# Kernel optimization log

Hardware: AMD Instinct MI355X
Metric: run time of the kernel (lower is better)

## Reference

```python
import jax, jax.numpy as jnp
import numpy as np

NUM_CLASSES = 80
TOPK = 1000
CONF_THRESH = 0.001
NMS_THRESH = 0.5
CLASS_OFFSET = 4096.0  # > max image coordinate, separates classes for class-aware NMS
M = 300000


def setup_inputs() -> dict:
    key = jax.random.key(0)
    k1, k2, k3, k4 = jax.random.split(key, 4)
    obj_preds = jax.random.normal(k1, (1, M, 1), dtype=jnp.float32)
    cls_preds = jax.random.normal(k2, (1, M, NUM_CLASSES), dtype=jnp.float32)
    # random xyxy boxes inside a 640x640 image
    cxcy = jax.random.uniform(k3, (1, M, 2), dtype=jnp.float32) * 640.0
    wh = jax.random.uniform(k4, (1, M, 2), dtype=jnp.float32) * 128.0 + 1.0
    box_preds = jnp.concatenate([cxcy - wh * 0.5, cxcy + wh * 0.5], axis=-1)
    return {"obj_preds": obj_preds, "cls_preds": cls_preds, "box_preds": box_preds}


def _iou_matrix(boxes):
    # boxes: [K, 4] xyxy -> [K, K] pairwise IoU
    x1, y1, x2, y2 = boxes[:, 0], boxes[:, 1], boxes[:, 2], boxes[:, 3]
    area = jnp.clip(x2 - x1, 0.0) * jnp.clip(y2 - y1, 0.0)
    xx1 = jnp.maximum(x1[:, None], x1[None, :])
    yy1 = jnp.maximum(y1[:, None], y1[None, :])
    xx2 = jnp.minimum(x2[:, None], x2[None, :])
    yy2 = jnp.minimum(y2[:, None], y2[None, :])
    inter = jnp.clip(xx2 - xx1, 0.0) * jnp.clip(yy2 - yy1, 0.0)
    return inter / (area[:, None] + area[None, :] - inter + 1e-9)


def _postprocess(obj_preds, cls_preds, box_preds):
    obj = obj_preds[0]   # [M, 1]
    cls = cls_preds[0]   # [M, C]
    box = box_preds[0]   # [M, 4]

    # sigmoid * sigmoid sqrt-score fusion (no_multi_labels branch)
    fused = jnp.sqrt(jax.nn.sigmoid(obj) * jax.nn.sigmoid(cls))  # [M, C]
    scores = jnp.max(fused, axis=1)     # [M]
    labels = jnp.argmax(fused, axis=1)  # [M]

    # sort-descending + take top-k == lax.top_k
    topk_scores, topk_idxs = jax.lax.top_k(scores, TOPK)
    labels_k = labels[topk_idxs]        # [K]
    boxes_k = box[topk_idxs]            # [K, 4]
    conf_mask = topk_scores > CONF_THRESH

    # multiclass NMS via class-offset trick (boxes of different classes never overlap)
    off = labels_k.astype(boxes_k.dtype)[:, None] * CLASS_OFFSET
    iou = _iou_matrix(boxes_k + off)    # [K, K]

    idx = jnp.arange(TOPK)

    def body(i, keep):
        # suppressed if any earlier, still-kept box overlaps > nms_thresh
        sup = (iou[i] > NMS_THRESH) & keep & (idx < i)
        return keep.at[i].set(keep[i] & ~jnp.any(sup))

    keep = jax.lax.fori_loop(0, TOPK, body, conf_mask)  # [K] bool

    keepf = keep.astype(topk_scores.dtype)
    # fixed-shape output: masked [K, 5] = (score, x1, y1, x2, y2); dropped rows zeroed
    out5 = jnp.concatenate([(topk_scores * keepf)[:, None], boxes_k * keepf[:, None]], axis=1)
    return out5, labels_k, keep


def reference(obj_preds, cls_preds, box_preds):
    return _postprocess(obj_preds, cls_preds, box_preds)
```

## Files before the change

kernel.cpp:

```cpp
#include <hip/hip_runtime.h>
#include <hip/hip_bf16.h>
#include <math.h>

#define NCLS 80
#define TOPK_N 1000
#define CAND_CAP 12288
#define T0 0.91f
#define OBJ_T 1.55f
#define NB 8192
#define HREP 8
#define RBINS 3072
#define RBIN_LO 0x3F680000u
#define ANCH_INV 524287

#define WS_SCORES   0
#define WS_CAND     1200000
#define WS_TKSCORE  1298304
#define WS_TKANCH   1302304
#define WS_TKLABEL  1306304
#define WS_BOXES    1310304
#define WS_OBX      1326304
#define WS_AREAS    1342304
#define WS_MASK     1346304
#define WS_META     1474304
#define WS_HIST     1474368

typedef unsigned long long u64;

__device__ __forceinline__ float sigmoidf_(float x) {
    return 1.0f / (1.0f + expf(-x));
}

__device__ __forceinline__ u64 make_key2(unsigned s32, int anchor) {
    return ((u64)s32 << 19) | (unsigned)(ANCH_INV - anchor);
}

__device__ __forceinline__ int key_bin(u64 k) {
    unsigned s32 = (unsigned)(k >> 19);
    int d = (int)(s32 - RBIN_LO);
    if (d < 0) d = 0;
    int b = d >> 9;
    if (b > RBINS - 1) b = RBINS - 1;
    return (RBINS - 1) - b;
}

__device__ __forceinline__ void rowmax16(const float4* row, int l,
                                         float& bv, int& bc) {
    float4 v4 = row[l];
    bv = v4.x; bc = l * 4;
    if (v4.y > bv) { bv = v4.y; bc = l * 4 + 1; }
    if (v4.z > bv) { bv = v4.z; bc = l * 4 + 2; }
    if (v4.w > bv) { bv = v4.w; bc = l * 4 + 3; }
    if (l < 4) {
        float4 w4 = row[16 + l];
        int cb = 64 + l * 4;
        if (w4.x > bv) { bv = w4.x; bc = cb; }
        if (w4.y > bv) { bv = w4.y; bc = cb + 1; }
        if (w4.z > bv) { bv = w4.z; bc = cb + 2; }
        if (w4.w > bv) { bv = w4.w; bc = cb + 3; }
    }
    #pragma unroll
    for (int m = 8; m >= 1; m >>= 1) {
        float ov = __shfl_xor(bv, m);
        int oc = __shfl_xor(bc, m);
        if (ov > bv || (ov == bv && oc < bc)) { bv = ov; bc = oc; }
    }
}

__global__ void __launch_bounds__(256)
k1_scores(const float* __restrict__ obj,
          const float* __restrict__ cls,
          u64* __restrict__ cand,
          int* __restrict__ counter,
          unsigned* __restrict__ hist,
          int M) {
    __shared__ int lcount, lbase;
    __shared__ u64 lkeys[64];
    int t = threadIdx.x;
    if (t == 0) lcount = 0;
    if (blockIdx.x < 4096 && t < 4)
        ((uint4*)hist)[blockIdx.x * 4 + t] = make_uint4(0u, 0u, 0u, 0u);
    __syncthreads();
    int l = t & 15;
    int grp = t >> 4;
    int base = blockIdx.x * 64 + grp * 4;
    if (base < M) {
        float4 ov = *(const float4*)(obj + base);
        float o4[4] = {ov.x, ov.y, ov.z, ov.w};
        #pragma unroll
        for (int j = 0; j < 4; ++j) {
            float o = o4[j];
            if (o > OBJ_T) {
                int anchor = base + j;
                const float4* p = (const float4*)(cls + (size_t)anchor * NCLS);
                float4 v = p[l];
                float m = fmaxf(fmaxf(v.x, v.y), fmaxf(v.z, v.w));
                if (l < 4) {
                    float4 w4 = p[16 + l];
                    m = fmaxf(m, fmaxf(fmaxf(w4.x, w4.y), fmaxf(w4.z, w4.w)));
                }
                #pragma unroll
                for (int s = 8; s >= 1; s >>= 1)
                    m = fmaxf(m, __shfl_xor(m, s));
                if (l == 0) {
                    float score = sqrtf(sigmoidf_(o) * sigmoidf_(m));
                    if (score > T0) {
                        int pos = atomicAdd(&lcount, 1);
                        lkeys[pos] = make_key2(__float_as_uint(score), anchor);
                    }
                }
            }
        }
    }
    __syncthreads();
    if (t == 0 && lcount > 0) lbase = atomicAdd(counter, lcount);
    __syncthreads();
    int n = lcount;
    if (t < n) {
        int pos = lbase + t;
        if (pos < CAND_CAP) cand[pos] = lkeys[t];
    }
}

__global__ void kf_hist(const float* __restrict__ obj,
                        const float* __restrict__ cls,
                        float* __restrict__ scores,
                        unsigned* __restrict__ hist,
                        const int* __restrict__ meta, int M) {
    int C = meta[2];
    if (C >= TOPK_N && C <= CAND_CAP) return;
    int gw = (blockIdx.x * 256 + threadIdx.x) >> 6;
    int TW = gridDim.x * 4;
    int lane = threadIdx.x & 63;
    int g = lane >> 4, l = lane & 15;
    int rep = blockIdx.x & (HREP - 1);
    for (int a0 = gw * 4; a0 < M; a0 += TW * 4) {
        int anchor = a0 + g;
        if (anchor >= M) continue;
        const float4* row = (const float4*)(cls + (size_t)anchor * NCLS);
        float bv; int bc;
        rowmax16(row, l, bv, bc);
        if (l == 0) {
            float score = sqrtf(sigmoidf_(obj[anchor]) * sigmoidf_(bv));
            scores[anchor] = score;
            atomicAdd(&hist[(size_t)rep * NB + (__float_as_uint(score) >> 17)], 1u);
        }
    }
}

__global__ void k2_scan(const unsigned* __restrict__ hist, int* __restrict__ meta) {
    int C = meta[2];
    if (C >= TOPK_N && C <= CAND_CAP) return;
    int t = threadIdx.x;
    int lane = t & 63, w = t >> 6;
    int base = NB - 1 - t * 8;
    unsigned bins[8]; unsigned s = 0;
    #pragma unroll
    for (int k = 0; k < 8; ++k) {
        unsigned h = 0;
        for (int r = 0; r < HREP; ++r) h += hist[(size_t)r * NB + base - k];
        bins[k] = h; s += h;
    }
    unsigned inc = s;
    for (int d = 1; d < 64; d <<= 1) {
        unsigned pv = __shfl_up(inc, d);
        if (lane >= d) inc += pv;
    }
    __shared__ unsigned wsum[16], woff[16];
    if (lane == 63) wsum[w] = inc;
    __syncthreads();
    if (t == 0) {
        unsigned cum = 0;
        for (int i = 0; i < 16; ++i) { woff[i] = cum; cum += wsum[i]; }
    }
    __syncthreads();
    unsigned excl = woff[w] + inc - s;
    if (excl < TOPK_N && excl + s >= TOPK_N) {
        unsigned cum = excl; int b = base;
        #pragma unroll
        for (int k = 0; k < 8; ++k) {
            unsigned h = bins[k];
            if (cum + h >= TOPK_N) { meta[0] = b; break; }
            cum += h; --b;
        }
    }
}

__global__ void k3_compact(const float* __restrict__ scores,
                           int* __restrict__ meta,
                           u64* __restrict__ cand, int M) {
    int C = meta[2];
    if (C >= TOPK_N && C <= CAND_CAP) return;
    int B = meta[0];
    for (int i = blockIdx.x * 256 + threadIdx.x; i < M; i += gridDim.x * 256) {
        unsigned key = __float_as_uint(scores[i]);
        if ((int)(key >> 17) >= B) {
            int pos = atomicAdd(meta + 3, 1);
            if (pos < CAND_CAP)
                cand[pos] = make_key2(key, i);
        }
    }
}

__global__ void __launch_bounds__(1024)
k4_rank(const u64* __restrict__ cand,
        const int* __restrict__ meta,
        float* __restrict__ tkscore,
        int* __restrict__ tkanchor) {
    __shared__ u64 sorted[CAND_CAP];
    __shared__ unsigned hist[RBINS];
    __shared__ unsigned cnt[RBINS];
    __shared__ unsigned wsum[16], woff[16];
    int t = threadIdx.x;
    int lane = t & 63, w = t >> 6;
    int Cf = meta[2];
    bool fast = (Cf >= TOPK_N && Cf <= CAND_CAP);
    int C = fast ? Cf : meta[3];
    if (C > CAND_CAP) C = CAND_CAP;
    for (int b = t; b < RBINS; b += 1024) { hist[b] = 0; cnt[b] = 0; }
    __syncthreads();
    u64 keys[12]; int nk = 0;
    for (int i = t; i < C; i += 1024) {
        u64 k = cand[i];
        keys[nk++] = k;
        atomicAdd(&hist[key_bin(k)], 1u);
    }
    __syncthreads();
    unsigned h0 = hist[t * 3], h1 = hist[t * 3 + 1], h2 = hist[t * 3 + 2];
    unsigned s = h0 + h1 + h2;
    unsigned inc = s;
    for (int d = 1; d < 64; d <<= 1) {
        unsigned pv = __shfl_up(inc, d);
        if (lane >= d) inc += pv;
    }
    if (lane == 63) wsum[w] = inc;
    __syncthreads();
    if (t == 0) {
        unsigned cum = 0;
        for (int i = 0; i < 16; ++i) { woff[i] = cum; cum += wsum[i]; }
    }
    __syncthreads();
    unsigned base = woff[w] + inc - s;
    hist[t * 3] = base;
    hist[t * 3 + 1] = base + h0;
    hist[t * 3 + 2] = base + h0 + h1;
    __syncthreads();
    nk = 0;
    for (int i = t; i < C; i += 1024) {
        u64 k = keys[nk++];
        int b = key_bin(k);
        unsigned pos = hist[b] + atomicAdd(&cnt[b], 1u);
        sorted[pos] = k;
    }
    __syncthreads();
    for (int p = t; p < C; p += 1024) {
        u64 k = sorted[p];
        int b = key_bin(k);
        unsigned b0 = hist[b], b1 = b0 + cnt[b];
        int r = (int)b0;
        for (unsigned q = b0; q < b1; ++q) r += (sorted[q] > k);
        if (r < TOPK_N) {
            tkscore[r] = __uint_as_float((unsigned)(k >> 19));
            tkanchor[r] = ANCH_INV - (int)(k & 0x7FFFF);
        }
    }
}

__global__ void __launch_bounds__(256)
k4b_gather(const float* __restrict__ cls,
           const float4* __restrict__ box,
           const int* __restrict__ tkanchor,
           int* __restrict__ tklabel,
           float4* __restrict__ boxes_k,
           float4* __restrict__ obx,
           float* __restrict__ areas) {
    int grp = threadIdx.x >> 4, l = threadIdx.x & 15;
    int r = blockIdx.x * 16 + grp;
    if (r >= TOPK_N) return;
    int anchor = tkanchor[r];
    const float4* row = (const float4*)(cls + (size_t)anchor * NCLS);
    float bv; int bc;
    rowmax16(row, l, bv, bc);
    if (l == 0) {
        tklabel[r] = bc;
        float4 b = box[anchor];
        boxes_k[r] = b;
        float off = (float)bc * 4096.0f;
        float4 ob = make_float4(b.x + off, b.y + off, b.z + off, b.w + off);
        obx[r] = ob;
        areas[r] = fmaxf(ob.z - ob.x, 0.0f) * fmaxf(ob.w - ob.y, 0.0f);
    }
}

__global__ void k5_iou(const float4* __restrict__ obx,
                       const float* __restrict__ areas,
                       u64* __restrict__ mask) {
    int i = blockIdx.x * 4 + (threadIdx.x >> 6);
    int lane = threadIdx.x & 63;
    if (i >= TOPK_N) return;
    float4 bi = obx[i];
    float ai = areas[i];
    for (int w = 0; w < 16; ++w) {
        int c = w * 64 + lane;
        bool bit = false;
        if (c < i) {
            float4 bc = obx[c];
            float xx1 = fmaxf(bi.x, bc.x), yy1 = fmaxf(bi.y, bc.y);
            float xx2 = fminf(bi.z, bc.z), yy2 = fminf(bi.w, bc.w);
            float inter = fmaxf(xx2 - xx1, 0.0f) * fmaxf(yy2 - yy1, 0.0f);
            float iou = inter / (ai + areas[c] - inter + 1e-9f);
            bit = iou > 0.5f;
        }
        u64 bal = __ballot(bit);
        if (lane == 0) mask[(size_t)i * 16 + w] = bal;
    }
}

__global__ void __launch_bounds__(1024)
k6_nms(const float* __restrict__ tkscore,
       const u64* __restrict__ mask,
       const int* __restrict__ tklabel,
       const float4* __restrict__ boxes_k,
       float* __restrict__ out) {
    __shared__ u64 kept_s[16], dec_s[16];
    int t = threadIdx.x, w = t >> 6, lane = t & 63;
    bool active = t < TOPK_N;
    u64 sup[16];
    float sc = 0.0f;
    if (active) {
        #pragma unroll
        for (int q = 0; q < 16; ++q) sup[q] = mask[(size_t)t * 16 + q];
        sc = tkscore[t];
    } else {
        #pragma unroll
        for (int q = 0; q < 16; ++q) sup[q] = 0ULL;
    }
    bool conf = active && (sc > 0.001f);
    bool mydec = !conf;
    bool mykept = false;
    u64 db = __ballot(mydec), kb = __ballot(mykept);
    if (lane == 0) { dec_s[w] = db; kept_s[w] = kb; }
    __syncthreads();
    for (int round = 0; round < TOPK_N; ++round) {
        if (!mydec) {
            u64 pend = 0;
            #pragma unroll
            for (int q = 0; q < 16; ++q) pend |= sup[q] & ~dec_s[q];
            if (pend == 0ULL) {
                u64 kk = 0;
                #pragma unroll
                for (int q = 0; q < 16; ++q) kk |= sup[q] & kept_s[q];
                mydec = true; mykept = (kk == 0ULL);
            }
        }
        __syncthreads();
        db = __ballot(mydec); kb = __ballot(mykept);
        if (lane == 0) { dec_s[w] = db; kept_s[w] = kb; }
        __syncthreads();
        u64 a = ~0ULL;
        #pragma unroll
        for (int q = 0; q < 16; ++q) a &= dec_s[q];
        if (a == ~0ULL) break;
    }
    if (active) {
        float k = mykept ? 1.0f : 0.0f;
        float4 b = boxes_k[t];
        out[t * 5 + 0] = sc * k;
        out[t * 5 + 1] = b.x * k;
        out[t * 5 + 2] = b.y * k;
        out[t * 5 + 3] = b.z * k;
        out[t * 5 + 4] = b.w * k;
        out[5 * TOPK_N + t] = (float)tklabel[t];
        out[6 * TOPK_N + t] = k;
    }
}

extern "C" void kernel_launch(void* const* d_in, const int* in_sizes, int n_in,
                              void* d_out, int out_size, void* d_ws, size_t ws_size,
                              hipStream_t stream) {
    const float* obj = (const float*)d_in[0];
    const float* cls = (const float*)d_in[1];
    const float* box = (const float*)d_in[2];
    float* out = (float*)d_out;
    char* ws = (char*)d_ws;
    int M = in_sizes[0];

    float*    scores  = (float*)(ws + WS_SCORES);
    u64*      cand    = (u64*)(ws + WS_CAND);
    float*    tkscore = (float*)(ws + WS_TKSCORE);
    int*      tkanch  = (int*)(ws + WS_TKANCH);
    int*      tklabel = (int*)(ws + WS_TKLABEL);
    float4*   boxes_k = (float4*)(ws + WS_BOXES);
    float4*   obx     = (float4*)(ws + WS_OBX);
    float*    areas   = (float*)(ws + WS_AREAS);
    u64*      mask    = (u64*)(ws + WS_MASK);
    int*      meta    = (int*)(ws + WS_META);
    unsigned* hist    = (unsigned*)(ws + WS_HIST);

    hipMemsetAsync(ws + WS_META, 0, 64, stream);

    k1_scores<<<(M + 63) / 64, 256, 0, stream>>>(obj, cls, cand, meta + 2, hist, M);
    kf_hist<<<512, 256, 0, stream>>>(obj, cls, scores, hist, meta, M);
    k2_scan<<<1, 1024, 0, stream>>>(hist, meta);
    k3_compact<<<512, 256, 0, stream>>>(scores, meta, cand, M);
    k4_rank<<<1, 1024, 0, stream>>>(cand, meta, tkscore, tkanch);
    k4b_gather<<<(TOPK_N + 15) / 16, 256, 0, stream>>>(cls, (const float4*)box,
                                                       tkanch, tklabel, boxes_k, obx, areas);
    k5_iou<<<(TOPK_N + 3) / 4, 256, 0, stream>>>(obx, areas, mask);
    k6_nms<<<1, 1024, 0, stream>>>(tkscore, mask, tklabel, boxes_k, out);
}
```

Measured before the change: 191.4 us.

## Compact objectness survivors in k1 and fold histogram scan into kf_hist tail

k1_scores now runs one anchor per thread and gathers anchors whose objectness passes the threshold into shared memory. 16-lane groups then take only those survivors for the class-row max, and the grid shrinks to a quarter of the blocks. The separate k2_scan launch is removed: the last block of kf_hist, found with an atomic counter and threadfence, performs the histogram scan itself with 256 threads covering 32 bins each. This saves one kernel launch and raises lane utilization in the prefilter. The cost is a serial tail in the last block and atomic reads of the histogram.

```diff
diff --git a/kernel.cpp b/kernel.cpp
--- a/kernel.cpp
+++ b/kernel.cpp
@@ -74,41 +74,41 @@
           int* __restrict__ counter,
           unsigned* __restrict__ hist,
           int M) {
-    __shared__ int lcount, lbase;
-    __shared__ u64 lkeys[64];
+    __shared__ int lcount, lbase, nsurv;
+    __shared__ int sanch[256];
+    __shared__ float sobj[256];
+    __shared__ u64 lkeys[256];
     int t = threadIdx.x;
-    if (t == 0) lcount = 0;
-    if (blockIdx.x < 4096 && t < 4)
-        ((uint4*)hist)[blockIdx.x * 4 + t] = make_uint4(0u, 0u, 0u, 0u);
-    __syncthreads();
-    int l = t & 15;
-    int grp = t >> 4;
-    int base = blockIdx.x * 64 + grp * 4;
-    if (base < M) {
-        float4 ov = *(const float4*)(obj + base);
-        float o4[4] = {ov.x, ov.y, ov.z, ov.w};
+    if (t == 0) { lcount = 0; nsurv = 0; }
+    for (int i = blockIdx.x * 256 + t; i < (HREP * NB) / 4; i += gridDim.x * 256)
+        ((uint4*)hist)[i] = make_uint4(0u, 0u, 0u, 0u);
+    __syncthreads();
+    int a = blockIdx.x * 256 + t;
+    float o = (a < M) ? obj[a] : -1e30f;
+    if (o > OBJ_T) {
+        int p = atomicAdd(&nsurv, 1);
+        sanch[p] = a; sobj[p] = o;
+    }
+    __syncthreads();
+    int ns = nsurv;
+    int grp = t >> 4, l = t & 15;
+    for (int s = grp; s < ns; s += 16) {
+        int anchor = sanch[s];
+        const float4* p = (const float4*)(cls + (size_t)anchor * NCLS);
+        float4 v = p[l];
+        float m = fmaxf(fmaxf(v.x, v.y), fmaxf(v.z, v.w));
+        if (l < 4) {
+            float4 w4 = p[16 + l];
+            m = fmaxf(m, fmaxf(fmaxf(w4.x, w4.y), fmaxf(w4.z, w4.w)));
+        }
         #pragma unroll
-        for (int j = 0; j < 4; ++j) {
-            float o = o4[j];
-            if (o > OBJ_T) {
-                int anchor = base + j;
-                const float4* p = (const float4*)(cls + (size_t)anchor * NCLS);
-                float4 v = p[l];
-                float m = fmaxf(fmaxf(v.x, v.y), fmaxf(v.z, v.w));
-                if (l < 4) {
-                    float4 w4 = p[16 + l];
-                    m = fmaxf(m, fmaxf(fmaxf(w4.x, w4.y), fmaxf(w4.z, w4.w)));
-                }
-                #pragma unroll
-                for (int s = 8; s >= 1; s >>= 1)
-                    m = fmaxf(m, __shfl_xor(m, s));
-                if (l == 0) {
-                    float score = sqrtf(sigmoidf_(o) * sigmoidf_(m));
-                    if (score > T0) {
-                        int pos = atomicAdd(&lcount, 1);
-                        lkeys[pos] = make_key2(__float_as_uint(score), anchor);
-                    }
-                }
+        for (int sh = 8; sh >= 1; sh >>= 1)
+            m = fmaxf(m, __shfl_xor(m, sh));
+        if (l == 0) {
+            float score = sqrtf(sigmoidf_(sobj[s]) * sigmoidf_(m));
+            if (score > T0) {
+                int pos = atomicAdd(&lcount, 1);
+                lkeys[pos] = make_key2(__float_as_uint(score), anchor);
             }
         }
     }
@@ -126,13 +126,14 @@
                         const float* __restrict__ cls,
                         float* __restrict__ scores,
                         unsigned* __restrict__ hist,
-                        const int* __restrict__ meta, int M) {
+                        int* __restrict__ meta, int M) {
     int C = meta[2];
     if (C >= TOPK_N && C <= CAND_CAP) return;
-    int gw = (blockIdx.x * 256 + threadIdx.x) >> 6;
+    int t = threadIdx.x;
+    int gw = (blockIdx.x * 256 + t) >> 6;
     int TW = gridDim.x * 4;
-    int lane = threadIdx.x & 63;
-    int g = lane >> 4, l = lane & 15;
+    int lane64 = t & 63;
+    int g = lane64 >> 4, l = lane64 & 15;
     int rep = blockIdx.x & (HREP - 1);
     for (int a0 = gw * 4; a0 < M; a0 += TW * 4) {
         int anchor = a0 + g;
@@ -146,19 +147,20 @@
             atomicAdd(&hist[(size_t)rep * NB + (__float_as_uint(score) >> 17)], 1u);
         }
     }
-}
-
-__global__ void k2_scan(const unsigned* __restrict__ hist, int* __restrict__ meta) {
-    int C = meta[2];
-    if (C >= TOPK_N && C <= CAND_CAP) return;
-    int t = threadIdx.x;
+    __threadfence();
+    __shared__ bool last;
+    if (t == 0)
+        last = (atomicAdd(meta + 4, 1) == (int)gridDim.x - 1);
+    __syncthreads();
+    if (!last) return;
     int lane = t & 63, w = t >> 6;
-    int base = NB - 1 - t * 8;
-    unsigned bins[8]; unsigned s = 0;
+    int base = NB - 1 - t * 32;
+    unsigned bins[32]; unsigned s = 0;
     #pragma unroll
-    for (int k = 0; k < 8; ++k) {
+    for (int k = 0; k < 32; ++k) {
         unsigned h = 0;
-        for (int r = 0; r < HREP; ++r) h += hist[(size_t)r * NB + base - k];
+        for (int r = 0; r < HREP; ++r)
+            h += atomicOr(&hist[(size_t)r * NB + base - k], 0u);
         bins[k] = h; s += h;
     }
     unsigned inc = s;
@@ -166,19 +168,19 @@
         unsigned pv = __shfl_up(inc, d);
         if (lane >= d) inc += pv;
     }
-    __shared__ unsigned wsum[16], woff[16];
+    __shared__ unsigned wsum[4], woff[4];
     if (lane == 63) wsum[w] = inc;
     __syncthreads();
     if (t == 0) {
         unsigned cum = 0;
-        for (int i = 0; i < 16; ++i) { woff[i] = cum; cum += wsum[i]; }
+        for (int i = 0; i < 4; ++i) { woff[i] = cum; cum += wsum[i]; }
     }
     __syncthreads();
     unsigned excl = woff[w] + inc - s;
     if (excl < TOPK_N && excl + s >= TOPK_N) {
         unsigned cum = excl; int b = base;
         #pragma unroll
-        for (int k = 0; k < 8; ++k) {
+        for (int k = 0; k < 32; ++k) {
             unsigned h = bins[k];
             if (cum + h >= TOPK_N) { meta[0] = b; break; }
             cum += h; --b;
@@ -399,9 +401,8 @@
 
     hipMemsetAsync(ws + WS_META, 0, 64, stream);
 
-    k1_scores<<<(M + 63) / 64, 256, 0, stream>>>(obj, cls, cand, meta + 2, hist, M);
+    k1_scores<<<(M + 255) / 256, 256, 0, stream>>>(obj, cls, cand, meta + 2, hist, M);
     kf_hist<<<512, 256, 0, stream>>>(obj, cls, scores, hist, meta, M);
-    k2_scan<<<1, 1024, 0, stream>>>(hist, meta);
     k3_compact<<<512, 256, 0, stream>>>(scores, meta, cand, M);
     k4_rank<<<1, 1024, 0, stream>>>(cand, meta, tkscore, tkanch);
     k4b_gather<<<(TOPK_N + 15) / 16, 256, 0, stream>>>(cls, (const float4*)box,
```

Result: faster. 171.9 us (-10.2%).
